# Kernel tuning notes

Measured on AMD Instinct MI355X. Metric: run time of the kernel, lower is better.

Reference implementation:

```python
import jax, jax.numpy as jnp
import numpy as np

N, E, D, H = 100000, 1600000, 32, 32


def setup_inputs() -> dict:
    key = jax.random.key(0)
    k1, k2, k3, k4 = jax.random.split(key, 4)
    x = jax.random.normal(k1, (N, D), dtype=jnp.float32)
    edge_index = jax.random.randint(k2, (2, E), 0, N, dtype=jnp.int64)
    W1 = jax.random.normal(k3, (D, H), dtype=jnp.float32) * (1.0 / np.sqrt(D))
    b1 = jnp.zeros((H,), dtype=jnp.float32)
    W2 = jax.random.normal(k4, (H, H), dtype=jnp.float32) * (1.0 / np.sqrt(H))
    b2 = jnp.zeros((H,), dtype=jnp.float32)
    return {"x": x, "edge_index": edge_index, "W1": W1, "b1": b1, "W2": W2, "b2": b2}


def _gcn_conv(x, src, dst, norm, W, b, n_nodes):
    # h = x W  ->  gather at src, scale by sym-norm, scatter-add at dst, + bias
    h = x @ W                                   # [N, H]
    msg = h[src] * norm[:, None]                # [E+N, H]
    out = jax.ops.segment_sum(msg, dst, num_segments=n_nodes)
    return out + b


def reference(x, edge_index, W1, b1, W2, b2):
    n = x.shape[0]
    loops = jnp.arange(n, dtype=edge_index.dtype)
    src = jnp.concatenate([edge_index[0], loops])  # source nodes (+ self loops)
    dst = jnp.concatenate([edge_index[1], loops])  # target nodes (+ self loops)
    # symmetric normalization: deg^{-1/2}[src] * deg^{-1/2}[dst] on A + I
    deg = jax.ops.segment_sum(jnp.ones_like(dst, dtype=x.dtype), dst, num_segments=n)
    dis = jnp.where(deg > 0, jax.lax.rsqrt(jnp.maximum(deg, 1e-12)), 0.0)
    norm = dis[src] * dis[dst]
    # layer 1: GCNConv -> ReLU (dropout is identity in eval mode)
    h = jax.nn.relu(_gcn_conv(x, src, dst, norm, W1, b1, n))
    # layer 2
    h = jax.nn.relu(_gcn_conv(h, src, dst, norm, W2, b2, n))
    return h
```

## Files before the change

### kernel.cpp

```cpp
#include <hip/hip_runtime.h>
#include <hip/hip_fp16.h>

#define FEAT 32
#define BIN_NODES 128
#define BIN_SHIFT 7
#define TILE_EDGES 8192
#define BWAVES 16
#define SRC_BITS 20
#define SRC_MASK 0xFFFFF
#define STAGE_CAP 6144

__device__ __forceinline__ int block_detect_int64(const int* __restrict__ raw32, int* nz) {
    if (threadIdx.x == 0) *nz = 0;
    __syncthreads();
    if (raw32[2 * threadIdx.x + 1] != 0) *nz = 1;
    __syncthreads();
    return (*nz == 0) ? 1 : 0;
}

__device__ __forceinline__ int load_idx(const void* raw, int f, long long i) {
    return f ? (int)((const long long*)raw)[i] : ((const int*)raw)[i];
}

__global__ __launch_bounds__(1024)
void binA_kernel(const void* __restrict__ raw, int* __restrict__ mat, int e, int nb) {
    extern __shared__ int hist[];
    int t = threadIdx.x;
    for (int i = t; i < BWAVES * nb; i += 1024) hist[i] = 0;
    int f = block_detect_int64((const int*)raw, &hist[BWAVES * nb]);
    int w = t >> 6, lane = t & 63;
    long long base = (long long)blockIdx.x * TILE_EDGES;
    int cnt = (int)min((long long)TILE_EDGES, (long long)e - base);
    int* hw = hist + w * nb;
    const int seg = TILE_EDGES / BWAVES;
    int wbeg = w * seg;
    int wend = min(wbeg + seg, cnt);
    for (int i = wbeg + lane; i < wend; i += 64) {
        int d = load_idx(raw, f, (long long)e + base + i);
        atomicAdd(&hw[d >> BIN_SHIFT], 1);
    }
    __syncthreads();
    for (int b = t; b < nb; b += 1024) {
        int s = 0;
#pragma unroll
        for (int w2 = 0; w2 < BWAVES; ++w2) s += hist[w2 * nb + b];
        mat[blockIdx.x * nb + b] = s;
    }
}

__device__ __forceinline__ int l2p(int L, int nb, int nblk) {
    int b = L / nblk;
    int k = L - b * nblk;
    return k * nb + b;
}

__global__ void scan1_kernel(int* __restrict__ mat, int* __restrict__ bsum,
                             int M, int nb, int nblk) {
    __shared__ int sd[256];
    int t = threadIdx.x;
    int L = blockIdx.x * 256 + t;
    int p = 0, v = 0;
    if (L < M) { p = l2p(L, nb, nblk); v = mat[p]; }
    sd[t] = v;
    __syncthreads();
    for (int off = 1; off < 256; off <<= 1) {
        int add = (t >= off) ? sd[t - off] : 0;
        __syncthreads();
        sd[t] += add;
        __syncthreads();
    }
    if (L < M) mat[p] = sd[t] - v;
    if (t == 255) bsum[blockIdx.x] = sd[t];
}

__global__ void scan2_kernel(int* __restrict__ bsum, int nbks) {
    __shared__ int sd[1024];
    int t = threadIdx.x;
    int v = (t < nbks) ? bsum[t] : 0;
    sd[t] = v;
    __syncthreads();
    for (int off = 1; off < 1024; off <<= 1) {
        int add = (t >= off) ? sd[t - off] : 0;
        __syncthreads();
        sd[t] += add;
        __syncthreads();
    }
    if (t < nbks) bsum[t] = sd[t] - v;
}

__global__ __launch_bounds__(1024)
void binC_kernel(const void* __restrict__ raw, const int* __restrict__ mat,
                 const int* __restrict__ bsum, int* __restrict__ packed,
                 int e, int nb, int nblk) {
    extern __shared__ int cur[];
    int t = threadIdx.x;
    int f = block_detect_int64((const int*)raw, &cur[nb]);
    for (int i = t; i < nb; i += 1024)
        cur[i] = mat[blockIdx.x * nb + i] + bsum[(i * nblk + blockIdx.x) >> 8];
    __syncthreads();
    long long base = (long long)blockIdx.x * TILE_EDGES;
    int cnt = (int)min((long long)TILE_EDGES, (long long)e - base);
    for (int i = t; i < cnt; i += 1024) {
        long long ei = base + i;
        int s = load_idx(raw, f, ei);
        int d = load_idx(raw, f, (long long)e + ei);
        int b = d >> BIN_SHIFT;
        int pos = atomicAdd(&cur[b], 1);
        packed[pos] = s | ((d & (BIN_NODES - 1)) << SRC_BITS);
    }
}

__global__ __launch_bounds__(1024)
void degsort_kernel(const int* __restrict__ packed, const int* __restrict__ mat,
                    const int* __restrict__ bsum, float* __restrict__ dis,
                    int* __restrict__ row_start, int* __restrict__ recs,
                    const float* __restrict__ x, const float* __restrict__ W1,
                    __half* __restrict__ h1,
                    int e, int n, int nb, int nblk) {
    __shared__ int cnt[BWAVES][BIN_NODES];
    __shared__ int wcur[BWAVES][BIN_NODES];
    __shared__ int exc[BIN_NODES];
    __shared__ float sdis[BIN_NODES];
    __shared__ float W1l[FEAT * FEAT];
    __shared__ int stage[STAGE_CAP];
    int b = blockIdx.x, t = threadIdx.x;
    int w = t >> 6;
    for (int i = t; i < BWAVES * BIN_NODES; i += 1024) ((int*)cnt)[i] = 0;
    if (t < FEAT * FEAT) W1l[t] = W1[t];
    __syncthreads();
    int start = mat[b] + bsum[(b * nblk) >> 8];
    int end = (b + 1 < nb) ? (mat[b + 1] + bsum[((b + 1) * nblk) >> 8]) : e;
    int m = end - start;
    if (m <= STAGE_CAP) {
        for (int i = t; i < m; i += 1024) {
            int rec = packed[start + i];
            stage[i] = rec;
            atomicAdd(&cnt[w][rec >> SRC_BITS], 1);
        }
    } else {
        for (int i = start + t; i < end; i += 1024)
            atomicAdd(&cnt[w][packed[i] >> SRC_BITS], 1);
    }
    __syncthreads();
    if (t < BIN_NODES) {
        int s = 0;
#pragma unroll
        for (int w2 = 0; w2 < BWAVES; ++w2) s += cnt[w2][t];
        exc[t] = s;
    }
    __syncthreads();
    for (int off = 1; off < BIN_NODES; off <<= 1) {
        int v = 0;
        if (t < BIN_NODES && t >= off) v = exc[t - off];
        __syncthreads();
        if (t < BIN_NODES) exc[t] += v;
        __syncthreads();
    }
    if (t < BIN_NODES) {
        int tot = 0;
#pragma unroll
        for (int w2 = 0; w2 < BWAVES; ++w2) tot += cnt[w2][t];
        int rs = start + exc[t] - tot;
        int run = rs;
#pragma unroll
        for (int w2 = 0; w2 < BWAVES; ++w2) { wcur[w2][t] = run; run += cnt[w2][t]; }
        float dv = rsqrtf((float)tot + 1.0f);
        sdis[t] = dv;
        int node = b * BIN_NODES + t;
        if (node < n) {
            dis[node] = dv;
            row_start[node] = rs;
        }
    }
    if (b == 0 && t == 128) row_start[n] = e;
    __syncthreads();
    if (m <= STAGE_CAP) {
        for (int i = t; i < m; i += 1024) {
            int rec = stage[i];
            int pos = atomicAdd(&wcur[w][rec >> SRC_BITS], 1);
            recs[pos] = rec & SRC_MASK;
        }
    } else {
        for (int i = start + t; i < end; i += 1024) {
            int rec = packed[i];
            int pos = atomicAdd(&wcur[w][rec >> SRC_BITS], 1);
            recs[pos] = rec & SRC_MASK;
        }
    }
    {
        int ln = b * BIN_NODES + (t >> 3);
        if (ln < n) {
            int q = t & 7;
            float4 xv = ((const float4*)x)[(size_t)ln * 8 + q];
            float xr[4] = {xv.x, xv.y, xv.z, xv.w};
            float o[4] = {0.f, 0.f, 0.f, 0.f};
#pragma unroll
            for (int k = 0; k < FEAT; ++k) {
                float xk = __shfl(xr[k & 3], k >> 2, 8);
#pragma unroll
                for (int c = 0; c < 4; ++c)
                    o[c] = fmaf(xk, W1l[k * FEAT + q * 4 + c], o[c]);
            }
            float dn = sdis[t >> 3];
            __half2* hp = (__half2*)&h1[(size_t)ln * FEAT + q * 4];
            hp[0] = __halves2half2(__float2half(dn * o[0]), __float2half(dn * o[1]));
            hp[1] = __halves2half2(__float2half(dn * o[2]), __float2half(dn * o[3]));
        }
    }
}

__global__ __launch_bounds__(256, 8)
void pull_mm_kernel(const int* __restrict__ recs, const int* __restrict__ row_start,
                    const __half* __restrict__ h, const float* __restrict__ dis,
                    const float* __restrict__ bias, const float* __restrict__ W2,
                    __half* __restrict__ h2, int n) {
    __shared__ float Wl[FEAT * FEAT];
    int t = threadIdx.x;
    for (int i = t; i < FEAT * FEAT; i += 256) {
        int k = i >> 5, j = i & 31;
        int col = (j & 24) | ((j + 2 * (k >> 3)) & 7);
        Wl[k * FEAT + col] = W2[i];
    }
    __syncthreads();
    int node = blockIdx.x * 16 + (t >> 4);
    if (node >= n) return;
    int g = t & 15;
    int sub = g >> 2;
    int fb = g & 3;
    int start = row_start[node];
    int deg = row_start[node + 1] - start;
    const float4* h4 = (const float4*)h;
    float s0 = 0, s1 = 0, s2 = 0, s3 = 0, s4 = 0, s5 = 0, s6 = 0, s7 = 0;
    for (int r0 = 0; r0 < deg; r0 += 32) {
#pragma unroll
        for (int w = 0; w < 8; ++w) {
            int r = r0 + w * 4 + sub;
            if (r < deg) {
                int s = recs[start + r];
                float4 v = h4[(size_t)s * 4 + fb];
                const __half2* hp = (const __half2*)&v;
                float2 a = __half22float2(hp[0]);
                float2 b = __half22float2(hp[1]);
                float2 c = __half22float2(hp[2]);
                float2 d = __half22float2(hp[3]);
                s0 += a.x; s1 += a.y; s2 += b.x; s3 += b.y;
                s4 += c.x; s5 += c.y; s6 += d.x; s7 += d.y;
            }
        }
    }
#pragma unroll
    for (int m = 4; m <= 8; m <<= 1) {
        s0 += __shfl_xor(s0, m, 64); s1 += __shfl_xor(s1, m, 64);
        s2 += __shfl_xor(s2, m, 64); s3 += __shfl_xor(s3, m, 64);
        s4 += __shfl_xor(s4, m, 64); s5 += __shfl_xor(s5, m, 64);
        s6 += __shfl_xor(s6, m, 64); s7 += __shfl_xor(s7, m, 64);
    }
    float dn = dis[node];
    float4 hv = h4[(size_t)node * 4 + fb];
    const __half2* hp = (const __half2*)&hv;
    float2 a = __half22float2(hp[0]);
    float2 b = __half22float2(hp[1]);
    float2 c = __half22float2(hp[2]);
    float2 d = __half22float2(hp[3]);
    const float4* bv4 = (const float4*)bias;
    float4 b0 = bv4[fb * 2], b1 = bv4[fb * 2 + 1];
    float o[8];
    o[0] = fmaxf(fmaf(dn, s0 + a.x, b0.x), 0.0f);
    o[1] = fmaxf(fmaf(dn, s1 + a.y, b0.y), 0.0f);
    o[2] = fmaxf(fmaf(dn, s2 + b.x, b0.z), 0.0f);
    o[3] = fmaxf(fmaf(dn, s3 + b.y, b0.w), 0.0f);
    o[4] = fmaxf(fmaf(dn, s4 + c.x, b1.x), 0.0f);
    o[5] = fmaxf(fmaf(dn, s5 + c.y, b1.y), 0.0f);
    o[6] = fmaxf(fmaf(dn, s6 + d.x, b1.z), 0.0f);
    o[7] = fmaxf(fmaf(dn, s7 + d.y, b1.w), 0.0f);
    float part[8] = {0.f, 0.f, 0.f, 0.f, 0.f, 0.f, 0.f, 0.f};
    const float* wrow = &Wl[(fb * 8) * FEAT + sub * 8];
#pragma unroll
    for (int cc = 0; cc < 8; ++cc) {
#pragma unroll
        for (int c2 = 0; c2 < 8; ++c2)
            part[c2] = fmaf(o[cc], wrow[cc * FEAT + ((c2 + 2 * fb) & 7)], part[c2]);
    }
#pragma unroll
    for (int m = 1; m <= 2; m <<= 1) {
        part[0] += __shfl_xor(part[0], m, 64); part[1] += __shfl_xor(part[1], m, 64);
        part[2] += __shfl_xor(part[2], m, 64); part[3] += __shfl_xor(part[3], m, 64);
        part[4] += __shfl_xor(part[4], m, 64); part[5] += __shfl_xor(part[5], m, 64);
        part[6] += __shfl_xor(part[6], m, 64); part[7] += __shfl_xor(part[7], m, 64);
    }
    if (fb == 0) {
        __half2 p0 = __halves2half2(__float2half(dn * part[0]), __float2half(dn * part[1]));
        __half2 p1 = __halves2half2(__float2half(dn * part[2]), __float2half(dn * part[3]));
        __half2 p2 = __halves2half2(__float2half(dn * part[4]), __float2half(dn * part[5]));
        __half2 p3 = __halves2half2(__float2half(dn * part[6]), __float2half(dn * part[7]));
        float4 pk;
        ((__half2*)&pk)[0] = p0; ((__half2*)&pk)[1] = p1;
        ((__half2*)&pk)[2] = p2; ((__half2*)&pk)[3] = p3;
        ((float4*)h2)[(size_t)node * 4 + sub] = pk;
    }
}

__global__ __launch_bounds__(256, 8)
void pull_kernel(const int* __restrict__ recs, const int* __restrict__ row_start,
                 const __half* __restrict__ h, const float* __restrict__ dis,
                 const float* __restrict__ bias, float* __restrict__ out, int n) {
    int t = threadIdx.x;
    int node = blockIdx.x * 16 + (t >> 4);
    if (node >= n) return;
    int g = t & 15;
    int sub = g >> 2;
    int fb = g & 3;
    int start = row_start[node];
    int deg = row_start[node + 1] - start;
    const float4* h4 = (const float4*)h;
    float s0 = 0, s1 = 0, s2 = 0, s3 = 0, s4 = 0, s5 = 0, s6 = 0, s7 = 0;
    for (int r0 = 0; r0 < deg; r0 += 32) {
#pragma unroll
        for (int w = 0; w < 8; ++w) {
            int r = r0 + w * 4 + sub;
            if (r < deg) {
                int s = recs[start + r];
                float4 v = h4[(size_t)s * 4 + fb];
                const __half2* hp = (const __half2*)&v;
                float2 a = __half22float2(hp[0]);
                float2 b = __half22float2(hp[1]);
                float2 c = __half22float2(hp[2]);
                float2 d = __half22float2(hp[3]);
                s0 += a.x; s1 += a.y; s2 += b.x; s3 += b.y;
                s4 += c.x; s5 += c.y; s6 += d.x; s7 += d.y;
            }
        }
    }
#pragma unroll
    for (int m = 4; m <= 8; m <<= 1) {
        s0 += __shfl_xor(s0, m, 64); s1 += __shfl_xor(s1, m, 64);
        s2 += __shfl_xor(s2, m, 64); s3 += __shfl_xor(s3, m, 64);
        s4 += __shfl_xor(s4, m, 64); s5 += __shfl_xor(s5, m, 64);
        s6 += __shfl_xor(s6, m, 64); s7 += __shfl_xor(s7, m, 64);
    }
    if (sub == 0) {
        float dn = dis[node];
        float4 hv = h4[(size_t)node * 4 + fb];
        const __half2* hp = (const __half2*)&hv;
        float2 a = __half22float2(hp[0]);
        float2 b = __half22float2(hp[1]);
        float2 c = __half22float2(hp[2]);
        float2 d = __half22float2(hp[3]);
        const float4* bv4 = (const float4*)bias;
        float4 b0 = bv4[fb * 2], b1 = bv4[fb * 2 + 1];
        float4 o0, o1;
        o0.x = fmaxf(fmaf(dn, s0 + a.x, b0.x), 0.0f);
        o0.y = fmaxf(fmaf(dn, s1 + a.y, b0.y), 0.0f);
        o0.z = fmaxf(fmaf(dn, s2 + b.x, b0.z), 0.0f);
        o0.w = fmaxf(fmaf(dn, s3 + b.y, b0.w), 0.0f);
        o1.x = fmaxf(fmaf(dn, s4 + c.x, b1.x), 0.0f);
        o1.y = fmaxf(fmaf(dn, s5 + c.y, b1.y), 0.0f);
        o1.z = fmaxf(fmaf(dn, s6 + d.x, b1.z), 0.0f);
        o1.w = fmaxf(fmaf(dn, s7 + d.y, b1.w), 0.0f);
        ((float4*)out)[(size_t)node * 8 + fb * 2] = o0;
        ((float4*)out)[(size_t)node * 8 + fb * 2 + 1] = o1;
    }
}

extern "C" void kernel_launch(void* const* d_in, const int* in_sizes, int n_in,
                              void* d_out, int out_size, void* d_ws, size_t ws_size,
                              hipStream_t stream) {
    const float* x = (const float*)d_in[0];
    const void* eidx_raw = d_in[1];
    const float* W1 = (const float*)d_in[2];
    const float* b1 = (const float*)d_in[3];
    const float* W2 = (const float*)d_in[4];
    const float* b2 = (const float*)d_in[5];
    float* out = (float*)d_out;

    const int n = in_sizes[0] / FEAT;
    const int e = in_sizes[1] / 2;
    const int nb = (n + BIN_NODES - 1) / BIN_NODES;
    const int nblk = (e + TILE_EDGES - 1) / TILE_EDGES;
    const int M = nb * nblk;
    const int nbks = (M + 255) / 256;

    char* ws = (char*)d_ws;
    size_t off = 0;
    auto alloc = [&](size_t bytes) { char* p = ws + off; off = (off + bytes + 255) & ~(size_t)255; return p; };
    int*    mat       = (int*)   alloc((size_t)M * 4);
    int*    bsum      = (int*)   alloc((size_t)nbks * 4);
    float*  dis       = (float*) alloc((size_t)n * 4);
    int*    row_start = (int*)   alloc((size_t)(n + 1) * 4);
    int*    recs      = (int*)   alloc((size_t)e * 4);
    __half* h1        = (__half*)alloc((size_t)n * FEAT * 2);
    __half* h2        = (__half*)alloc((size_t)(n * FEAT * 2 > e * 4 ? (size_t)n * FEAT * 2 : (size_t)e * 4));
    int*    packed    = (int*)h2;

    const size_t ldsA = (size_t)(BWAVES * nb + 1) * 4;
    const size_t ldsC = (size_t)(nb + 1) * 4;
    const int gNode = (n + 15) / 16;

    binA_kernel<<<nblk, 1024, ldsA, stream>>>(eidx_raw, mat, e, nb);
    scan1_kernel<<<nbks, 256, 0, stream>>>(mat, bsum, M, nb, nblk);
    scan2_kernel<<<1, 1024, 0, stream>>>(bsum, nbks);
    binC_kernel<<<nblk, 1024, ldsC, stream>>>(eidx_raw, mat, bsum, packed, e, nb, nblk);
    degsort_kernel<<<nb, 1024, 0, stream>>>(packed, mat, bsum, dis, row_start,
                                            recs, x, W1, h1, e, n, nb, nblk);

    pull_mm_kernel<<<gNode, 256, 0, stream>>>(recs, row_start, h1, dis, b1, W2, h2, n);
    pull_kernel<<<gNode, 256, 0, stream>>>(recs, row_start, h2, dis, b2, out, n);
}
```

Baseline: 183.3 us.

## Fuse graph preprocessing into one cooperative kernel and narrow pull groups

The five CSR-build kernels (histogram, two scans, binning, per-bin sort with the first matmul) are merged into one cooperative kernel that separates phases with grid.sync. Each thread keeps its edge src/dst values in registers between the histogram and scatter phases, so the edge list is read once instead of twice. Per-bin sorting now loops over bins across the fixed grid. Separately, both aggregation kernels drop from 16 to 8 lanes per node, which changes the reduction and W2 tiling (padded 33-wide LDS rows). The cost is grid-wide barriers, a grid limited to co-resident blocks, and fewer lanes hiding gather latency per node.

```diff
diff --git a/kernel.cpp b/kernel.cpp
--- a/kernel.cpp
+++ b/kernel.cpp
@@ -1,5 +1,8 @@
 #include <hip/hip_runtime.h>
 #include <hip/hip_fp16.h>
+#include <hip/hip_cooperative_groups.h>
+
+namespace cg = cooperative_groups;
 
 #define FEAT 32
 #define BIN_NODES 128
@@ -10,42 +13,8 @@
 #define SRC_MASK 0xFFFFF
 #define STAGE_CAP 6144
 
-__device__ __forceinline__ int block_detect_int64(const int* __restrict__ raw32, int* nz) {
-    if (threadIdx.x == 0) *nz = 0;
-    __syncthreads();
-    if (raw32[2 * threadIdx.x + 1] != 0) *nz = 1;
-    __syncthreads();
-    return (*nz == 0) ? 1 : 0;
-}
-
 __device__ __forceinline__ int load_idx(const void* raw, int f, long long i) {
     return f ? (int)((const long long*)raw)[i] : ((const int*)raw)[i];
-}
-
-__global__ __launch_bounds__(1024)
-void binA_kernel(const void* __restrict__ raw, int* __restrict__ mat, int e, int nb) {
-    extern __shared__ int hist[];
-    int t = threadIdx.x;
-    for (int i = t; i < BWAVES * nb; i += 1024) hist[i] = 0;
-    int f = block_detect_int64((const int*)raw, &hist[BWAVES * nb]);
-    int w = t >> 6, lane = t & 63;
-    long long base = (long long)blockIdx.x * TILE_EDGES;
-    int cnt = (int)min((long long)TILE_EDGES, (long long)e - base);
-    int* hw = hist + w * nb;
-    const int seg = TILE_EDGES / BWAVES;
-    int wbeg = w * seg;
-    int wend = min(wbeg + seg, cnt);
-    for (int i = wbeg + lane; i < wend; i += 64) {
-        int d = load_idx(raw, f, (long long)e + base + i);
-        atomicAdd(&hw[d >> BIN_SHIFT], 1);
-    }
-    __syncthreads();
-    for (int b = t; b < nb; b += 1024) {
-        int s = 0;
-#pragma unroll
-        for (int w2 = 0; w2 < BWAVES; ++w2) s += hist[w2 * nb + b];
-        mat[blockIdx.x * nb + b] = s;
-    }
 }
 
 __device__ __forceinline__ int l2p(int L, int nb, int nblk) {
@@ -54,157 +23,194 @@
     return k * nb + b;
 }
 
-__global__ void scan1_kernel(int* __restrict__ mat, int* __restrict__ bsum,
-                             int M, int nb, int nblk) {
-    __shared__ int sd[256];
-    int t = threadIdx.x;
-    int L = blockIdx.x * 256 + t;
-    int p = 0, v = 0;
-    if (L < M) { p = l2p(L, nb, nblk); v = mat[p]; }
-    sd[t] = v;
+__global__ __launch_bounds__(1024, 4)
+void build_kernel(const void* __restrict__ raw, int* __restrict__ mat,
+                  int* __restrict__ bsum, int* __restrict__ packed,
+                  float* __restrict__ dis, int* __restrict__ row_start,
+                  int* __restrict__ recs, const float* __restrict__ x,
+                  const float* __restrict__ W1, __half* __restrict__ h1,
+                  int e, int n, int nb, int nblk, int nbks, int M) {
+    extern __shared__ int lds[];
+    cg::grid_group grid = cg::this_grid();
+    const int t = threadIdx.x, blk = blockIdx.x;
+    const int w = t >> 6;
+
+    const int nzoff = BWAVES * nb;
+    for (int i = t; i < BWAVES * nb; i += 1024) lds[i] = 0;
+    if (t == 0) lds[nzoff] = 0;
     __syncthreads();
-    for (int off = 1; off < 256; off <<= 1) {
-        int add = (t >= off) ? sd[t - off] : 0;
-        __syncthreads();
-        sd[t] += add;
-        __syncthreads();
-    }
-    if (L < M) mat[p] = sd[t] - v;
-    if (t == 255) bsum[blockIdx.x] = sd[t];
-}
-
-__global__ void scan2_kernel(int* __restrict__ bsum, int nbks) {
-    __shared__ int sd[1024];
-    int t = threadIdx.x;
-    int v = (t < nbks) ? bsum[t] : 0;
-    sd[t] = v;
+    if (((const int*)raw)[2 * t + 1] != 0) lds[nzoff] = 1;
     __syncthreads();
-    for (int off = 1; off < 1024; off <<= 1) {
-        int add = (t >= off) ? sd[t - off] : 0;
-        __syncthreads();
-        sd[t] += add;
-        __syncthreads();
-    }
-    if (t < nbks) bsum[t] = sd[t] - v;
-}
-
-__global__ __launch_bounds__(1024)
-void binC_kernel(const void* __restrict__ raw, const int* __restrict__ mat,
-                 const int* __restrict__ bsum, int* __restrict__ packed,
-                 int e, int nb, int nblk) {
-    extern __shared__ int cur[];
-    int t = threadIdx.x;
-    int f = block_detect_int64((const int*)raw, &cur[nb]);
-    for (int i = t; i < nb; i += 1024)
-        cur[i] = mat[blockIdx.x * nb + i] + bsum[(i * nblk + blockIdx.x) >> 8];
+    const int f = (lds[nzoff] == 0) ? 1 : 0;
+    if (blk == 0 && t == 0) row_start[n] = e;
+
+    long long base = (long long)blk * TILE_EDGES;
+    int cnt_e = (int)min((long long)TILE_EDGES, (long long)e - base);
+    int sreg[8], dreg[8];
+    int* hw = lds + w * nb;
+#pragma unroll
+    for (int k = 0; k < 8; ++k) {
+        int i = t + k * 1024;
+        if (i < cnt_e) {
+            sreg[k] = load_idx(raw, f, base + i);
+            dreg[k] = load_idx(raw, f, (long long)e + base + i);
+            atomicAdd(&hw[dreg[k] >> BIN_SHIFT], 1);
+        } else {
+            dreg[k] = -1;
+        }
+    }
     __syncthreads();
-    long long base = (long long)blockIdx.x * TILE_EDGES;
-    int cnt = (int)min((long long)TILE_EDGES, (long long)e - base);
-    for (int i = t; i < cnt; i += 1024) {
-        long long ei = base + i;
-        int s = load_idx(raw, f, ei);
-        int d = load_idx(raw, f, (long long)e + ei);
-        int b = d >> BIN_SHIFT;
-        int pos = atomicAdd(&cur[b], 1);
-        packed[pos] = s | ((d & (BIN_NODES - 1)) << SRC_BITS);
-    }
-}
-
-__global__ __launch_bounds__(1024)
-void degsort_kernel(const int* __restrict__ packed, const int* __restrict__ mat,
-                    const int* __restrict__ bsum, float* __restrict__ dis,
-                    int* __restrict__ row_start, int* __restrict__ recs,
-                    const float* __restrict__ x, const float* __restrict__ W1,
-                    __half* __restrict__ h1,
-                    int e, int n, int nb, int nblk) {
-    __shared__ int cnt[BWAVES][BIN_NODES];
-    __shared__ int wcur[BWAVES][BIN_NODES];
-    __shared__ int exc[BIN_NODES];
-    __shared__ float sdis[BIN_NODES];
-    __shared__ float W1l[FEAT * FEAT];
-    __shared__ int stage[STAGE_CAP];
-    int b = blockIdx.x, t = threadIdx.x;
-    int w = t >> 6;
-    for (int i = t; i < BWAVES * BIN_NODES; i += 1024) ((int*)cnt)[i] = 0;
-    if (t < FEAT * FEAT) W1l[t] = W1[t];
-    __syncthreads();
-    int start = mat[b] + bsum[(b * nblk) >> 8];
-    int end = (b + 1 < nb) ? (mat[b + 1] + bsum[((b + 1) * nblk) >> 8]) : e;
-    int m = end - start;
-    if (m <= STAGE_CAP) {
-        for (int i = t; i < m; i += 1024) {
-            int rec = packed[start + i];
-            stage[i] = rec;
-            atomicAdd(&cnt[w][rec >> SRC_BITS], 1);
-        }
-    } else {
-        for (int i = start + t; i < end; i += 1024)
-            atomicAdd(&cnt[w][packed[i] >> SRC_BITS], 1);
-    }
-    __syncthreads();
-    if (t < BIN_NODES) {
+    for (int b2 = t; b2 < nb; b2 += 1024) {
         int s = 0;
 #pragma unroll
-        for (int w2 = 0; w2 < BWAVES; ++w2) s += cnt[w2][t];
-        exc[t] = s;
-    }
-    __syncthreads();
-    for (int off = 1; off < BIN_NODES; off <<= 1) {
-        int v = 0;
-        if (t < BIN_NODES && t >= off) v = exc[t - off];
-        __syncthreads();
-        if (t < BIN_NODES) exc[t] += v;
-        __syncthreads();
-    }
-    if (t < BIN_NODES) {
-        int tot = 0;
-#pragma unroll
-        for (int w2 = 0; w2 < BWAVES; ++w2) tot += cnt[w2][t];
-        int rs = start + exc[t] - tot;
-        int run = rs;
-#pragma unroll
-        for (int w2 = 0; w2 < BWAVES; ++w2) { wcur[w2][t] = run; run += cnt[w2][t]; }
-        float dv = rsqrtf((float)tot + 1.0f);
-        sdis[t] = dv;
-        int node = b * BIN_NODES + t;
-        if (node < n) {
-            dis[node] = dv;
-            row_start[node] = rs;
-        }
-    }
-    if (b == 0 && t == 128) row_start[n] = e;
-    __syncthreads();
-    if (m <= STAGE_CAP) {
-        for (int i = t; i < m; i += 1024) {
-            int rec = stage[i];
-            int pos = atomicAdd(&wcur[w][rec >> SRC_BITS], 1);
-            recs[pos] = rec & SRC_MASK;
-        }
-    } else {
-        for (int i = start + t; i < end; i += 1024) {
-            int rec = packed[i];
-            int pos = atomicAdd(&wcur[w][rec >> SRC_BITS], 1);
-            recs[pos] = rec & SRC_MASK;
-        }
-    }
+        for (int w2 = 0; w2 < BWAVES; ++w2) s += lds[w2 * nb + b2];
+        mat[blk * nb + b2] = s;
+    }
+    __threadfence();
+    grid.sync();
+
     {
-        int ln = b * BIN_NODES + (t >> 3);
-        if (ln < n) {
-            int q = t & 7;
-            float4 xv = ((const float4*)x)[(size_t)ln * 8 + q];
-            float xr[4] = {xv.x, xv.y, xv.z, xv.w};
-            float o[4] = {0.f, 0.f, 0.f, 0.f};
-#pragma unroll
-            for (int k = 0; k < FEAT; ++k) {
-                float xk = __shfl(xr[k & 3], k >> 2, 8);
-#pragma unroll
-                for (int c = 0; c < 4; ++c)
-                    o[c] = fmaf(xk, W1l[k * FEAT + q * 4 + c], o[c]);
-            }
-            float dn = sdis[t >> 3];
-            __half2* hp = (__half2*)&h1[(size_t)ln * FEAT + q * 4];
-            hp[0] = __halves2half2(__float2half(dn * o[0]), __float2half(dn * o[1]));
-            hp[1] = __halves2half2(__float2half(dn * o[2]), __float2half(dn * o[3]));
+        int v = blk * 4 + (t >> 8);
+        int lt = t & 255;
+        int* sd = lds + (t >> 8) * 256;
+        int L = v * 256 + lt;
+        int p = 0, val = 0;
+        if (L < M) { p = l2p(L, nb, nblk); val = mat[p]; }
+        sd[lt] = val;
+        __syncthreads();
+        for (int off = 1; off < 256; off <<= 1) {
+            int add = (lt >= off) ? sd[lt - off] : 0;
+            __syncthreads();
+            sd[lt] += add;
+            __syncthreads();
+        }
+        if (L < M) mat[p] = sd[lt] - val;
+        if (lt == 255 && v < nbks) bsum[v] = sd[lt];
+    }
+    __threadfence();
+    grid.sync();
+
+    if (blk == 0) {
+        int v2 = (t < nbks) ? bsum[t] : 0;
+        lds[t] = v2;
+        __syncthreads();
+        for (int off = 1; off < 1024; off <<= 1) {
+            int add = (t >= off) ? lds[t - off] : 0;
+            __syncthreads();
+            lds[t] += add;
+            __syncthreads();
+        }
+        if (t < nbks) bsum[t] = lds[t] - v2;
+    }
+    __threadfence();
+    grid.sync();
+
+    {
+        int* cur = lds;
+        for (int i = t; i < nb; i += 1024)
+            cur[i] = mat[blk * nb + i] + bsum[(i * nblk + blk) >> 8];
+        __syncthreads();
+#pragma unroll
+        for (int k = 0; k < 8; ++k) {
+            int d = dreg[k];
+            if (d >= 0) {
+                int pos = atomicAdd(&cur[d >> BIN_SHIFT], 1);
+                packed[pos] = sreg[k] | ((d & (BIN_NODES - 1)) << SRC_BITS);
+            }
+        }
+    }
+    __threadfence();
+    grid.sync();
+
+    int* cntL  = lds;
+    int* wcurL = lds + 2048;
+    int* excL  = lds + 4096;
+    float* sdisL = (float*)(lds + 4224);
+    float* W1l   = (float*)(lds + 4352);
+    int* stageL  = lds + 5376;
+    W1l[t] = W1[t];
+
+    for (int b = blk; b < nb; b += nblk) {
+        __syncthreads();
+        for (int i = t; i < BWAVES * BIN_NODES; i += 1024) cntL[i] = 0;
+        __syncthreads();
+        int start = mat[b] + bsum[(b * nblk) >> 8];
+        int end = (b + 1 < nb) ? (mat[b + 1] + bsum[((b + 1) * nblk) >> 8]) : e;
+        int m = end - start;
+        if (m <= STAGE_CAP) {
+            for (int i = t; i < m; i += 1024) {
+                int rec = packed[start + i];
+                stageL[i] = rec;
+                atomicAdd(&cntL[w * BIN_NODES + (rec >> SRC_BITS)], 1);
+            }
+        } else {
+            for (int i = start + t; i < end; i += 1024)
+                atomicAdd(&cntL[w * BIN_NODES + (packed[i] >> SRC_BITS)], 1);
+        }
+        __syncthreads();
+        if (t < BIN_NODES) {
+            int s = 0;
+#pragma unroll
+            for (int w2 = 0; w2 < BWAVES; ++w2) s += cntL[w2 * BIN_NODES + t];
+            excL[t] = s;
+        }
+        __syncthreads();
+        for (int off = 1; off < BIN_NODES; off <<= 1) {
+            int v = 0;
+            if (t < BIN_NODES && t >= off) v = excL[t - off];
+            __syncthreads();
+            if (t < BIN_NODES) excL[t] += v;
+            __syncthreads();
+        }
+        if (t < BIN_NODES) {
+            int tot = 0;
+#pragma unroll
+            for (int w2 = 0; w2 < BWAVES; ++w2) tot += cntL[w2 * BIN_NODES + t];
+            int rs = start + excL[t] - tot;
+            int run = rs;
+#pragma unroll
+            for (int w2 = 0; w2 < BWAVES; ++w2) {
+                wcurL[w2 * BIN_NODES + t] = run;
+                run += cntL[w2 * BIN_NODES + t];
+            }
+            float dv = rsqrtf((float)tot + 1.0f);
+            sdisL[t] = dv;
+            int node = b * BIN_NODES + t;
+            if (node < n) { dis[node] = dv; row_start[node] = rs; }
+        }
+        __syncthreads();
+        if (m <= STAGE_CAP) {
+            for (int i = t; i < m; i += 1024) {
+                int rec = stageL[i];
+                int pos = atomicAdd(&wcurL[w * BIN_NODES + (rec >> SRC_BITS)], 1);
+                recs[pos] = rec & SRC_MASK;
+            }
+        } else {
+            for (int i = start + t; i < end; i += 1024) {
+                int rec = packed[i];
+                int pos = atomicAdd(&wcurL[w * BIN_NODES + (rec >> SRC_BITS)], 1);
+                recs[pos] = rec & SRC_MASK;
+            }
+        }
+        {
+            int ln = b * BIN_NODES + (t >> 3);
+            if (ln < n) {
+                int q = t & 7;
+                float4 xv = ((const float4*)x)[(size_t)ln * 8 + q];
+                float xr[4] = {xv.x, xv.y, xv.z, xv.w};
+                float o[4] = {0.f, 0.f, 0.f, 0.f};
+#pragma unroll
+                for (int k = 0; k < FEAT; ++k) {
+                    float xk = __shfl(xr[k & 3], k >> 2, 8);
+#pragma unroll
+                    for (int c = 0; c < 4; ++c)
+                        o[c] = fmaf(xk, W1l[k * FEAT + q * 4 + c], o[c]);
+                }
+                float dn = sdisL[t >> 3];
+                __half2* hp = (__half2*)&h1[(size_t)ln * FEAT + q * 4];
+                hp[0] = __halves2half2(__float2half(dn * o[0]), __float2half(dn * o[1]));
+                hp[1] = __halves2half2(__float2half(dn * o[2]), __float2half(dn * o[3]));
+            }
         }
     }
 }
@@ -214,27 +220,26 @@
                     const __half* __restrict__ h, const float* __restrict__ dis,
                     const float* __restrict__ bias, const float* __restrict__ W2,
                     __half* __restrict__ h2, int n) {
-    __shared__ float Wl[FEAT * FEAT];
+    __shared__ float Wl[FEAT * 33];
     int t = threadIdx.x;
     for (int i = t; i < FEAT * FEAT; i += 256) {
         int k = i >> 5, j = i & 31;
-        int col = (j & 24) | ((j + 2 * (k >> 3)) & 7);
-        Wl[k * FEAT + col] = W2[i];
+        Wl[k * 33 + j] = W2[i];
     }
     __syncthreads();
-    int node = blockIdx.x * 16 + (t >> 4);
+    int node = blockIdx.x * 32 + (t >> 3);
     if (node >= n) return;
-    int g = t & 15;
+    int g = t & 7;
     int sub = g >> 2;
     int fb = g & 3;
     int start = row_start[node];
     int deg = row_start[node + 1] - start;
     const float4* h4 = (const float4*)h;
     float s0 = 0, s1 = 0, s2 = 0, s3 = 0, s4 = 0, s5 = 0, s6 = 0, s7 = 0;
-    for (int r0 = 0; r0 < deg; r0 += 32) {
+    for (int r0 = 0; r0 < deg; r0 += 16) {
 #pragma unroll
         for (int w = 0; w < 8; ++w) {
-            int r = r0 + w * 4 + sub;
+            int r = r0 + w * 2 + sub;
             if (r < deg) {
                 int s = recs[start + r];
                 float4 v = h4[(size_t)s * 4 + fb];
@@ -248,13 +253,10 @@
             }
         }
     }
-#pragma unroll
-    for (int m = 4; m <= 8; m <<= 1) {
-        s0 += __shfl_xor(s0, m, 64); s1 += __shfl_xor(s1, m, 64);
-        s2 += __shfl_xor(s2, m, 64); s3 += __shfl_xor(s3, m, 64);
-        s4 += __shfl_xor(s4, m, 64); s5 += __shfl_xor(s5, m, 64);
-        s6 += __shfl_xor(s6, m, 64); s7 += __shfl_xor(s7, m, 64);
-    }
+    s0 += __shfl_xor(s0, 4, 64); s1 += __shfl_xor(s1, 4, 64);
+    s2 += __shfl_xor(s2, 4, 64); s3 += __shfl_xor(s3, 4, 64);
+    s4 += __shfl_xor(s4, 4, 64); s5 += __shfl_xor(s5, 4, 64);
+    s6 += __shfl_xor(s6, 4, 64); s7 += __shfl_xor(s7, 4, 64);
     float dn = dis[node];
     float4 hv = h4[(size_t)node * 4 + fb];
     const __half2* hp = (const __half2*)&hv;
@@ -273,30 +275,32 @@
     o[5] = fmaxf(fmaf(dn, s5 + c.y, b1.y), 0.0f);
     o[6] = fmaxf(fmaf(dn, s6 + d.x, b1.z), 0.0f);
     o[7] = fmaxf(fmaf(dn, s7 + d.y, b1.w), 0.0f);
-    float part[8] = {0.f, 0.f, 0.f, 0.f, 0.f, 0.f, 0.f, 0.f};
-    const float* wrow = &Wl[(fb * 8) * FEAT + sub * 8];
+    float part[16];
+#pragma unroll
+    for (int j = 0; j < 16; ++j) part[j] = 0.f;
+    const float* wrow = &Wl[(fb * 8) * 33 + sub * 16];
 #pragma unroll
     for (int cc = 0; cc < 8; ++cc) {
 #pragma unroll
-        for (int c2 = 0; c2 < 8; ++c2)
-            part[c2] = fmaf(o[cc], wrow[cc * FEAT + ((c2 + 2 * fb) & 7)], part[c2]);
+        for (int j = 0; j < 16; ++j)
+            part[j] = fmaf(o[cc], wrow[cc * 33 + j], part[j]);
     }
 #pragma unroll
     for (int m = 1; m <= 2; m <<= 1) {
-        part[0] += __shfl_xor(part[0], m, 64); part[1] += __shfl_xor(part[1], m, 64);
-        part[2] += __shfl_xor(part[2], m, 64); part[3] += __shfl_xor(part[3], m, 64);
-        part[4] += __shfl_xor(part[4], m, 64); part[5] += __shfl_xor(part[5], m, 64);
-        part[6] += __shfl_xor(part[6], m, 64); part[7] += __shfl_xor(part[7], m, 64);
+#pragma unroll
+        for (int j = 0; j < 16; ++j) part[j] += __shfl_xor(part[j], m, 64);
     }
     if (fb == 0) {
-        __half2 p0 = __halves2half2(__float2half(dn * part[0]), __float2half(dn * part[1]));
-        __half2 p1 = __halves2half2(__float2half(dn * part[2]), __float2half(dn * part[3]));
-        __half2 p2 = __halves2half2(__float2half(dn * part[4]), __float2half(dn * part[5]));
-        __half2 p3 = __halves2half2(__float2half(dn * part[6]), __float2half(dn * part[7]));
-        float4 pk;
-        ((__half2*)&pk)[0] = p0; ((__half2*)&pk)[1] = p1;
-        ((__half2*)&pk)[2] = p2; ((__half2*)&pk)[3] = p3;
-        ((float4*)h2)[(size_t)node * 4 + sub] = pk;
+        float4 pk0, pk1;
+#pragma unroll
+        for (int q = 0; q < 4; ++q) {
+            ((__half2*)&pk0)[q] = __halves2half2(__float2half(dn * part[2 * q]),
+                                                 __float2half(dn * part[2 * q + 1]));
+            ((__half2*)&pk1)[q] = __halves2half2(__float2half(dn * part[8 + 2 * q]),
+                                                 __float2half(dn * part[8 + 2 * q + 1]));
+        }
+        ((float4*)h2)[(size_t)node * 4 + sub * 2]     = pk0;
+        ((float4*)h2)[(size_t)node * 4 + sub * 2 + 1] = pk1;
     }
 }
 
@@ -305,19 +309,19 @@
                  const __half* __restrict__ h, const float* __restrict__ dis,
                  const float* __restrict__ bias, float* __restrict__ out, int n) {
     int t = threadIdx.x;
-    int node = blockIdx.x * 16 + (t >> 4);
+    int node = blockIdx.x * 32 + (t >> 3);
     if (node >= n) return;
-    int g = t & 15;
+    int g = t & 7;
     int sub = g >> 2;
     int fb = g & 3;
     int start = row_start[node];
     int deg = row_start[node + 1] - start;
     const float4* h4 = (const float4*)h;
     float s0 = 0, s1 = 0, s2 = 0, s3 = 0, s4 = 0, s5 = 0, s6 = 0, s7 = 0;
-    for (int r0 = 0; r0 < deg; r0 += 32) {
+    for (int r0 = 0; r0 < deg; r0 += 16) {
 #pragma unroll
         for (int w = 0; w < 8; ++w) {
-            int r = r0 + w * 4 + sub;
+            int r = r0 + w * 2 + sub;
             if (r < deg) {
                 int s = recs[start + r];
                 float4 v = h4[(size_t)s * 4 + fb];
@@ -331,13 +335,10 @@
             }
         }
     }
-#pragma unroll
-    for (int m = 4; m <= 8; m <<= 1) {
-        s0 += __shfl_xor(s0, m, 64); s1 += __shfl_xor(s1, m, 64);
-        s2 += __shfl_xor(s2, m, 64); s3 += __shfl_xor(s3, m, 64);
-        s4 += __shfl_xor(s4, m, 64); s5 += __shfl_xor(s5, m, 64);
-        s6 += __shfl_xor(s6, m, 64); s7 += __shfl_xor(s7, m, 64);
-    }
+    s0 += __shfl_xor(s0, 4, 64); s1 += __shfl_xor(s1, 4, 64);
+    s2 += __shfl_xor(s2, 4, 64); s3 += __shfl_xor(s3, 4, 64);
+    s4 += __shfl_xor(s4, 4, 64); s5 += __shfl_xor(s5, 4, 64);
+    s6 += __shfl_xor(s6, 4, 64); s7 += __shfl_xor(s7, 4, 64);
     if (sub == 0) {
         float dn = dis[node];
         float4 hv = h4[(size_t)node * 4 + fb];
@@ -373,12 +374,12 @@
     const float* b2 = (const float*)d_in[5];
     float* out = (float*)d_out;
 
-    const int n = in_sizes[0] / FEAT;
-    const int e = in_sizes[1] / 2;
-    const int nb = (n + BIN_NODES - 1) / BIN_NODES;
-    const int nblk = (e + TILE_EDGES - 1) / TILE_EDGES;
-    const int M = nb * nblk;
-    const int nbks = (M + 255) / 256;
+    int n = in_sizes[0] / FEAT;
+    int e = in_sizes[1] / 2;
+    int nb = (n + BIN_NODES - 1) / BIN_NODES;
+    int nblk = (e + TILE_EDGES - 1) / TILE_EDGES;
+    int M = nb * nblk;
+    int nbks = (M + 255) / 256;
 
     char* ws = (char*)d_ws;
     size_t off = 0;
@@ -392,16 +393,15 @@
     __half* h2        = (__half*)alloc((size_t)(n * FEAT * 2 > e * 4 ? (size_t)n * FEAT * 2 : (size_t)e * 4));
     int*    packed    = (int*)h2;
 
-    const size_t ldsA = (size_t)(BWAVES * nb + 1) * 4;
-    const size_t ldsC = (size_t)(nb + 1) * 4;
-    const int gNode = (n + 15) / 16;
-
-    binA_kernel<<<nblk, 1024, ldsA, stream>>>(eidx_raw, mat, e, nb);
-    scan1_kernel<<<nbks, 256, 0, stream>>>(mat, bsum, M, nb, nblk);
-    scan2_kernel<<<1, 1024, 0, stream>>>(bsum, nbks);
-    binC_kernel<<<nblk, 1024, ldsC, stream>>>(eidx_raw, mat, bsum, packed, e, nb, nblk);
-    degsort_kernel<<<nb, 1024, 0, stream>>>(packed, mat, bsum, dis, row_start,
-                                            recs, x, W1, h1, e, n, nb, nblk);
+    const size_t ldsB = (size_t)(BWAVES * nb + 1) * 4;
+    const int gNode = (n + 31) / 32;
+
+    void* args[] = {(void*)&eidx_raw, (void*)&mat, (void*)&bsum, (void*)&packed,
+                    (void*)&dis, (void*)&row_start, (void*)&recs, (void*)&x,
+                    (void*)&W1, (void*)&h1, (void*)&e, (void*)&n, (void*)&nb,
+                    (void*)&nblk, (void*)&nbks, (void*)&M};
+    hipLaunchCooperativeKernel((void*)build_kernel, dim3(nblk), dim3(1024),
+                               args, (unsigned int)ldsB, stream);
 
     pull_mm_kernel<<<gNode, 256, 0, stream>>>(recs, row_start, h1, dis, b1, W2, h2, n);
     pull_kernel<<<gNode, 256, 0, stream>>>(recs, row_start, h2, dis, b2, out, n);
```

After: 577.3 us. +214.9%, slower.
